# Kernel optimization log

Measured on AMD Instinct MI355X. Metric: run time of the kernel, lower is better.

The kernel has to match this reference:

```python
import jax, jax.numpy as jnp
import numpy as np

NUM_HEADS = 12
HEAD_DIM = 64
DIM = 768
ATTN_DIM = 768
SEQ = 4096


def _rotate_half(t):
    # split last dim in halves: (x1, x2) -> (-x2, x1)
    x1, x2 = jnp.split(t, 2, axis=-1)
    return jnp.concatenate([-x2, x1], axis=-1)


def _apply_rope(t, freqs):
    # t: [B,H,L,d], freqs: [1,1,L,d]
    return t * jnp.cos(freqs) + _rotate_half(t) * jnp.sin(freqs)


def setup_inputs() -> dict:
    key = jax.random.key(0)
    ks = jax.random.split(key, 8)
    x = jax.random.normal(ks[0], (1, SEQ, DIM), dtype=jnp.float32)
    # standard rotary frequencies: theta = pos * inv_freq, concatenated twice to head_dim
    inv_freq = 1.0 / (10000.0 ** (jnp.arange(0, HEAD_DIM, 2, dtype=jnp.float32) / HEAD_DIM))
    pos = jnp.arange(SEQ, dtype=jnp.float32)
    ang = pos[:, None] * inv_freq[None, :]                      # [L, d/2]
    rope = jnp.concatenate([ang, ang], axis=-1)[None, None]     # [1,1,L,d]
    s = 0.02
    Wq = jax.random.normal(ks[1], (ATTN_DIM, DIM), dtype=jnp.float32) * s
    Wk = jax.random.normal(ks[2], (ATTN_DIM, DIM), dtype=jnp.float32) * s
    Wv = jax.random.normal(ks[3], (ATTN_DIM, DIM), dtype=jnp.float32) * s
    Wo = jax.random.normal(ks[4], (DIM, ATTN_DIM), dtype=jnp.float32) * s
    bo = jnp.zeros((DIM,), dtype=jnp.float32)
    gamma = jnp.ones((DIM,), dtype=jnp.float32)
    beta = jnp.zeros((DIM,), dtype=jnp.float32)
    return {"x": x, "Wq": Wq, "Wk": Wk, "Wv": Wv, "Wo": Wo, "bo": bo,
            "gamma": gamma, "beta": beta, "rope": rope}


def reference(x, Wq, Wk, Wv, Wo, bo, gamma, beta, rope):
    B, L, D = x.shape
    residual = x
    # pre-LayerNorm
    mu = jnp.mean(x, axis=-1, keepdims=True)
    var = jnp.mean((x - mu) ** 2, axis=-1, keepdims=True)
    xn = (x - mu) * jax.lax.rsqrt(var + 1e-5) * gamma + beta

    def heads(t):  # [B,L,attn_dim] -> [B,H,L,d]
        return t.reshape(B, L, NUM_HEADS, HEAD_DIM).transpose(0, 2, 1, 3)

    q = heads(xn @ Wq.T)
    k = heads(xn @ Wk.T)
    v = heads(xn @ Wv.T)
    q = _apply_rope(q, rope)
    k = _apply_rope(k, rope)
    v = _apply_rope(v, rope)

    scale = HEAD_DIM ** -0.5
    dots = jnp.einsum('bhid,bhjd->bhij', q, k) * scale
    # causal mask: positions j > i masked
    i = jnp.arange(L)
    mask = i[:, None] < i[None, :]  # True where future
    neg = -jnp.finfo(dots.dtype).max
    dots = jnp.where(mask[None, None], neg, dots)
    attn_map = jax.nn.softmax(dots, axis=-1)

    o = jnp.einsum('bhij,bhjd->bhid', attn_map, v)
    o = o.transpose(0, 2, 1, 3).reshape(B, L, ATTN_DIM)
    out = o @ Wo.T + bo + residual
    return out, attn_map, dots
```

## Files before the change

### kernel.cpp

```cpp
#include <hip/hip_runtime.h>
#include <hip/hip_bf16.h>
#include <cfloat>
#include <cmath>

#define SEQ 4096
#define DIM 768
#define NH 12
#define HD 64
#define NEG_MASK (-0x1.FEp+127f)

typedef __attribute__((ext_vector_type(8))) short short8_t;
typedef __attribute__((ext_vector_type(4))) float f32x4;

static __device__ __forceinline__ unsigned short f2bf(float f) {
  __hip_bfloat16 h = __float2bfloat16(f);
  unsigned short u;
  __builtin_memcpy(&u, &h, 2);
  return u;
}

static __device__ __forceinline__ void st_nt(float* p, f32x4 v) {
  __builtin_nontemporal_store(v, (f32x4*)p);
}
static __device__ __forceinline__ f32x4 ld_lds4(const float* p) {
  return *(const f32x4*)p;
}

__global__ __launch_bounds__(256) void ln_kernel(const float* __restrict__ x,
    const float* __restrict__ gamma, const float* __restrict__ beta,
    unsigned short* __restrict__ xnb) {
  int row = blockIdx.x;
  const float* xr = x + (size_t)row * DIM;
  int t = threadIdx.x;
  float v0 = xr[t], v1 = xr[t + 256], v2 = xr[t + 512];
  float s = v0 + v1 + v2;
  float s2 = v0 * v0 + v1 * v1 + v2 * v2;
  for (int off = 32; off > 0; off >>= 1) {
    s += __shfl_down(s, off, 64);
    s2 += __shfl_down(s2, off, 64);
  }
  __shared__ float red[2][4];
  int wid = t >> 6;
  if ((t & 63) == 0) { red[0][wid] = s; red[1][wid] = s2; }
  __syncthreads();
  s = red[0][0] + red[0][1] + red[0][2] + red[0][3];
  s2 = red[1][0] + red[1][1] + red[1][2] + red[1][3];
  float mu = s * (1.0f / DIM);
  float var = s2 * (1.0f / DIM) - mu * mu;
  float rstd = rsqrtf(var + 1e-5f);
  unsigned short* xo = xnb + (size_t)row * DIM;
  xo[t]       = f2bf((v0 - mu) * rstd * gamma[t]       + beta[t]);
  xo[t + 256] = f2bf((v1 - mu) * rstd * gamma[t + 256] + beta[t + 256]);
  xo[t + 512] = f2bf((v2 - mu) * rstd * gamma[t + 512] + beta[t + 512]);
}

__global__ __launch_bounds__(256) void wcvt_kernel(const float* __restrict__ w0,
    const float* __restrict__ w1, const float* __restrict__ w2, const float* __restrict__ w3,
    unsigned short* __restrict__ o0, unsigned short* __restrict__ o1,
    unsigned short* __restrict__ o2, unsigned short* __restrict__ o3) {
  const float* src; unsigned short* dst;
  switch (blockIdx.y) {
    case 0: src = w0; dst = o0; break;
    case 1: src = w1; dst = o1; break;
    case 2: src = w2; dst = o2; break;
    default: src = w3; dst = o3; break;
  }
  size_t base = ((size_t)blockIdx.x * 256 + threadIdx.x) * 8;
  float4 a = *(const float4*)(src + base);
  float4 b = *(const float4*)(src + base + 4);
  ushort4 ua, ub;
  ua.x = f2bf(a.x); ua.y = f2bf(a.y); ua.z = f2bf(a.z); ua.w = f2bf(a.w);
  ub.x = f2bf(b.x); ub.y = f2bf(b.y); ub.z = f2bf(b.z); ub.w = f2bf(b.w);
  *(ushort4*)(dst + base) = ua;
  *(ushort4*)(dst + base + 4) = ub;
}

__global__ __launch_bounds__(256) void qkv_kernel(const unsigned short* __restrict__ xnb,
    const unsigned short* __restrict__ wqb, const unsigned short* __restrict__ wkb,
    const unsigned short* __restrict__ wvb, const float* __restrict__ ropes,
    unsigned short* __restrict__ qb, unsigned short* __restrict__ kb,
    unsigned short* __restrict__ vbT) {
  int z = blockIdx.z;
  const unsigned short* W = (z == 0) ? wqb : (z == 1) ? wkb : wvb;
  int h = blockIdx.y;
  int n0 = h * 64;
  int tid = threadIdx.x;
  int w = tid >> 6, l = tid & 63;
  int col_l = l & 15, rowg = l >> 4, kgrp = rowg * 8;
  int mbase = blockIdx.x * 64 + w * 16;

  f32x4 acc[4];
  #pragma unroll
  for (int g = 0; g < 4; g++) acc[g] = (f32x4){0.f, 0.f, 0.f, 0.f};

  for (int k0 = 0; k0 < DIM; k0 += 32) {
    short8_t a = *(const short8_t*)(xnb + (size_t)(mbase + col_l) * DIM + k0 + kgrp);
    #pragma unroll
    for (int g = 0; g < 4; g++) {
      short8_t bw = *(const short8_t*)(W + (size_t)(n0 + g * 16 + col_l) * DIM + k0 + kgrp);
      acc[g] = __builtin_amdgcn_mfma_f32_16x16x32_bf16(a, bw, acc[g], 0, 0, 0);
    }
  }

  float res[4][4];
  #pragma unroll
  for (int g = 0; g < 4; g++) {
    int d = g * 16 + col_l;
    #pragma unroll
    for (int r = 0; r < 4; r++) {
      int m = mbase + rowg * 4 + r;
      float f = ropes[(size_t)m * HD + d];
      float val = acc[g][r];
      float oth = acc[g ^ 2][r];
      float rot = (g < 2) ? -oth : oth;
      res[g][r] = val * cosf(f) + rot * sinf(f);
    }
  }

  if (z < 2) {
    unsigned short* dst = (z == 0) ? qb : kb;
    #pragma unroll
    for (int g = 0; g < 4; g++) {
      int d = g * 16 + col_l;
      #pragma unroll
      for (int r = 0; r < 4; r++)
        dst[((size_t)h * SEQ + mbase + rowg * 4 + r) * HD + d] = f2bf(res[g][r]);
    }
  } else {
    #pragma unroll
    for (int g = 0; g < 4; g++) {
      int d = g * 16 + col_l;
      ushort4 u;
      u.x = f2bf(res[g][0]); u.y = f2bf(res[g][1]);
      u.z = f2bf(res[g][2]); u.w = f2bf(res[g][3]);
      *(ushort4*)(vbT + ((size_t)h * HD + d) * SEQ + mbase + rowg * 4) = u;
    }
  }
}

__global__ __launch_bounds__(256, 4) void attn_fused(
    const unsigned short* __restrict__ qb, const unsigned short* __restrict__ kb,
    const unsigned short* __restrict__ vbT,
    float* __restrict__ dots, float* __restrict__ attnp, unsigned short* __restrict__ ob) {
  int band = (SEQ / 16 - 1) - blockIdx.x;
  int h = blockIdx.y;
  int i0 = band * 16;
  int jd = i0 >> 6;
  int tid = threadIdx.x;
  int w = tid >> 6, l = tid & 63;
  int col_l = l & 15, rg = l >> 4, kgrp = rg * 8;
  int c4 = col_l * 4;

  const unsigned short* qh = qb + (size_t)h * SEQ * HD;
  const unsigned short* kh = kb + (size_t)h * SEQ * HD;
  const unsigned short* vh = vbT + (size_t)h * HD * SEQ;
  size_t obase = (size_t)h * SEQ * SEQ;

  __shared__ float pt[4][16][68];
  __shared__ float stats[4][16][2];

  const unsigned short* qrow = qh + (size_t)(i0 + col_l) * HD + kgrp;
  short8_t aq0 = *(const short8_t*)(qrow);
  short8_t aq1 = *(const short8_t*)(qrow + 32);

  float mreg[4], lreg[4];
  #pragma unroll
  for (int r = 0; r < 4; r++) { mreg[r] = -FLT_MAX; lreg[r] = 0.f; }

  for (int jt = w; jt <= jd; jt += 4) {
    int j0 = jt * 64;
    f32x4 acc[4];
    #pragma unroll
    for (int b = 0; b < 4; b++) {
      const unsigned short* kr = kh + (size_t)(j0 + b * 16 + col_l) * HD + kgrp;
      short8_t bk0 = *(const short8_t*)(kr);
      short8_t bk1 = *(const short8_t*)(kr + 32);
      f32x4 z = {0.f, 0.f, 0.f, 0.f};
      acc[b] = __builtin_amdgcn_mfma_f32_16x16x32_bf16(aq0, bk0, z, 0, 0, 0);
      acc[b] = __builtin_amdgcn_mfma_f32_16x16x32_bf16(aq1, bk1, acc[b], 0, 0, 0);
    }
    bool diag = (jt == jd);
    #pragma unroll
    for (int b = 0; b < 4; b++) {
      int j = j0 + b * 16 + col_l;
      #pragma unroll
      for (int r = 0; r < 4; r++) {
        float s = acc[b][r] * 0.125f;
        acc[b][r] = (diag && j > i0 + rg * 4 + r) ? NEG_MASK : s;
      }
    }
    #pragma unroll
    for (int r = 0; r < 4; r++) {
      float tm = fmaxf(fmaxf(acc[0][r], acc[1][r]), fmaxf(acc[2][r], acc[3][r]));
      if (tm > -1e30f) {
        float nm = fmaxf(mreg[r], tm);
        lreg[r] = lreg[r] * __expf(mreg[r] - nm) +
                  __expf(acc[0][r] - nm) + __expf(acc[1][r] - nm) +
                  __expf(acc[2][r] - nm) + __expf(acc[3][r] - nm);
        mreg[r] = nm;
      }
    }
    #pragma unroll
    for (int b = 0; b < 4; b++)
      #pragma unroll
      for (int r = 0; r < 4; r++)
        pt[w][rg * 4 + r][b * 16 + col_l] = acc[b][r];
    #pragma unroll
    for (int e = 0; e < 4; e++) {
      f32x4 v = ld_lds4(&pt[w][e * 4 + rg][c4]);
      st_nt(dots + obase + (size_t)(i0 + e * 4 + rg) * SEQ + j0 + c4, v);
    }
  }

  #pragma unroll
  for (int r = 0; r < 4; r++) {
    float m = mreg[r], lv = lreg[r];
    #pragma unroll
    for (int off = 1; off < 16; off <<= 1) {
      float om = __shfl_xor(m, off, 16);
      float ol = __shfl_xor(lv, off, 16);
      float nm = fmaxf(m, om);
      lv = lv * __expf(m - nm) + ol * __expf(om - nm);
      m = nm;
    }
    mreg[r] = m; lreg[r] = lv;
  }
  if (col_l == 0) {
    #pragma unroll
    for (int r = 0; r < 4; r++) {
      stats[w][rg * 4 + r][0] = mreg[r];
      stats[w][rg * 4 + r][1] = lreg[r];
    }
  }
  __syncthreads();
  float M_[4], rl_[4];
  #pragma unroll
  for (int r = 0; r < 4; r++) {
    int row = rg * 4 + r;
    float m0 = stats[0][row][0], m1 = stats[1][row][0];
    float m2 = stats[2][row][0], m3 = stats[3][row][0];
    float mm = fmaxf(fmaxf(m0, m1), fmaxf(m2, m3));
    float L = stats[0][row][1] * __expf(m0 - mm) + stats[1][row][1] * __expf(m1 - mm) +
              stats[2][row][1] * __expf(m2 - mm) + stats[3][row][1] * __expf(m3 - mm);
    M_[r] = mm;
    rl_[r] = 1.0f / L;
  }

  f32x4 o[4];
  #pragma unroll
  for (int dg = 0; dg < 4; dg++) o[dg] = (f32x4){0.f, 0.f, 0.f, 0.f};

  for (int jt = w; jt <= jd; jt += 4) {
    int j0 = jt * 64;
    f32x4 acc[4];
    #pragma unroll
    for (int b = 0; b < 4; b++) {
      const unsigned short* kr = kh + (size_t)(j0 + b * 16 + col_l) * HD + kgrp;
      short8_t bk0 = *(const short8_t*)(kr);
      short8_t bk1 = *(const short8_t*)(kr + 32);
      f32x4 z = {0.f, 0.f, 0.f, 0.f};
      acc[b] = __builtin_amdgcn_mfma_f32_16x16x32_bf16(aq0, bk0, z, 0, 0, 0);
      acc[b] = __builtin_amdgcn_mfma_f32_16x16x32_bf16(aq1, bk1, acc[b], 0, 0, 0);
    }
    bool diag = (jt == jd);
    #pragma unroll
    for (int b = 0; b < 4; b++) {
      int j = j0 + b * 16 + col_l;
      #pragma unroll
      for (int r = 0; r < 4; r++) {
        float s = acc[b][r] * 0.125f;
        s = (diag && j > i0 + rg * 4 + r) ? NEG_MASK : s;
        float p = __expf(s - M_[r]) * rl_[r];
        pt[w][rg * 4 + r][b * 16 + col_l] = p;
      }
    }
    #pragma unroll
    for (int e = 0; e < 4; e++) {
      f32x4 v = ld_lds4(&pt[w][e * 4 + rg][c4]);
      st_nt(attnp + obase + (size_t)(i0 + e * 4 + rg) * SEQ + j0 + c4, v);
    }
    short8_t pa[2];
    #pragma unroll
    for (int ks = 0; ks < 2; ks++) {
      const float* src = &pt[w][col_l][ks * 32 + kgrp];
      f32x4 x0 = ld_lds4(src);
      f32x4 x1 = ld_lds4(src + 4);
      short8_t t;
      t[0] = (short)f2bf(x0.x); t[1] = (short)f2bf(x0.y);
      t[2] = (short)f2bf(x0.z); t[3] = (short)f2bf(x0.w);
      t[4] = (short)f2bf(x1.x); t[5] = (short)f2bf(x1.y);
      t[6] = (short)f2bf(x1.z); t[7] = (short)f2bf(x1.w);
      pa[ks] = t;
    }
    #pragma unroll
    for (int dg = 0; dg < 4; dg++) {
      const unsigned short* vr = vh + (size_t)(dg * 16 + col_l) * SEQ + j0 + kgrp;
      short8_t bv0 = *(const short8_t*)(vr);
      short8_t bv1 = *(const short8_t*)(vr + 32);
      o[dg] = __builtin_amdgcn_mfma_f32_16x16x32_bf16(pa[0], bv0, o[dg], 0, 0, 0);
      o[dg] = __builtin_amdgcn_mfma_f32_16x16x32_bf16(pa[1], bv1, o[dg], 0, 0, 0);
    }
  }

  {
    int c0 = (jd + 1) * 64;
    int nf4 = (SEQ - c0) >> 2;
    if (nf4 > 0) {
      f32x4 dm = (f32x4){NEG_MASK, NEG_MASK, NEG_MASK, NEG_MASK};
      f32x4 zz = (f32x4){0.f, 0.f, 0.f, 0.f};
      for (int r16 = 0; r16 < 16; r16++) {
        float* dr = dots  + obase + (size_t)(i0 + r16) * SEQ + c0;
        float* ar = attnp + obase + (size_t)(i0 + r16) * SEQ + c0;
        for (int c = tid; c < nf4; c += 256) {
          st_nt(dr + c * 4, dm);
          st_nt(ar + c * 4, zz);
        }
      }
    }
  }

  __syncthreads();
  #pragma unroll
  for (int dg = 0; dg < 4; dg++)
    #pragma unroll
    for (int r = 0; r < 4; r++)
      pt[w][rg * 4 + r][dg * 16 + col_l] = o[dg][r];
  __syncthreads();
  {
    int idx = tid * 4;
    int row = idx >> 6, col = idx & 63;
    f32x4 s = ld_lds4(&pt[0][row][col]);
    #pragma unroll
    for (int w2 = 1; w2 < 4; w2++) {
      f32x4 t = ld_lds4(&pt[w2][row][col]);
      s.x += t.x; s.y += t.y; s.z += t.z; s.w += t.w;
    }
    ushort4 u;
    u.x = f2bf(s.x); u.y = f2bf(s.y); u.z = f2bf(s.z); u.w = f2bf(s.w);
    *(ushort4*)(ob + (size_t)(i0 + row) * DIM + h * HD + col) = u;
  }
}

__global__ __launch_bounds__(256) void out_kernel(const unsigned short* __restrict__ ob,
    const unsigned short* __restrict__ wob, const float* __restrict__ bias,
    const float* __restrict__ resid, float* __restrict__ out) {
  int n0 = blockIdx.y * 64;
  int tid = threadIdx.x;
  int w = tid >> 6, l = tid & 63;
  int col_l = l & 15, rowg = l >> 4, kgrp = rowg * 8;
  int mbase = blockIdx.x * 64 + w * 16;

  f32x4 acc[4];
  #pragma unroll
  for (int g = 0; g < 4; g++) acc[g] = (f32x4){0.f, 0.f, 0.f, 0.f};

  for (int k0 = 0; k0 < DIM; k0 += 32) {
    short8_t a = *(const short8_t*)(ob + (size_t)(mbase + col_l) * DIM + k0 + kgrp);
    #pragma unroll
    for (int g = 0; g < 4; g++) {
      short8_t bw = *(const short8_t*)(wob + (size_t)(n0 + g * 16 + col_l) * DIM + k0 + kgrp);
      acc[g] = __builtin_amdgcn_mfma_f32_16x16x32_bf16(a, bw, acc[g], 0, 0, 0);
    }
  }
  #pragma unroll
  for (int g = 0; g < 4; g++) {
    int n = n0 + g * 16 + col_l;
    float bn = bias[n];
    #pragma unroll
    for (int r = 0; r < 4; r++) {
      int m = mbase + rowg * 4 + r;
      out[(size_t)m * DIM + n] = acc[g][r] + bn + resid[(size_t)m * DIM + n];
    }
  }
}

extern "C" void kernel_launch(void* const* d_in, const int* in_sizes, int n_in,
                              void* d_out, int out_size, void* d_ws, size_t ws_size,
                              hipStream_t stream) {
  const float* x     = (const float*)d_in[0];
  const float* Wq    = (const float*)d_in[1];
  const float* Wk    = (const float*)d_in[2];
  const float* Wv    = (const float*)d_in[3];
  const float* Wo    = (const float*)d_in[4];
  const float* bo    = (const float*)d_in[5];
  const float* gamma = (const float*)d_in[6];
  const float* beta  = (const float*)d_in[7];
  const float* rope  = (const float*)d_in[8];

  float* out  = (float*)d_out;
  float* attn = out + (size_t)SEQ * DIM;
  float* dots = attn + (size_t)NH * SEQ * SEQ;

  char* ws = (char*)d_ws;
  unsigned short* xnb = (unsigned short*)(ws);
  unsigned short* qb  = (unsigned short*)(ws + 6291456);
  unsigned short* kb  = (unsigned short*)(ws + 12582912);
  unsigned short* vbT = (unsigned short*)(ws + 18874368);
  unsigned short* ob  = (unsigned short*)(ws + 25165824);
  unsigned short* wqb = (unsigned short*)(ws + 31457280);
  unsigned short* wkb = (unsigned short*)(ws + 32636928);
  unsigned short* wvb = (unsigned short*)(ws + 33816576);
  unsigned short* wob = (unsigned short*)(ws + 34996224);

  ln_kernel<<<SEQ, 256, 0, stream>>>(x, gamma, beta, xnb);
  wcvt_kernel<<<dim3(288, 4), 256, 0, stream>>>(Wq, Wk, Wv, Wo, wqb, wkb, wvb, wob);
  qkv_kernel<<<dim3(SEQ / 64, NH, 3), 256, 0, stream>>>(xnb, wqb, wkb, wvb, rope, qb, kb, vbT);
  attn_fused<<<dim3(SEQ / 16, NH), 256, 0, stream>>>(qb, kb, vbT, dots, attn, ob);
  out_kernel<<<dim3(SEQ / 64, DIM / 64), 256, 0, stream>>>(ob, wob, bo, x, out);
}
```

Before: 563.7 us.

## Reuse stored dots in softmax pass instead of recomputing QK^T

The second pass no longer recomputes Q·K^T with MFMA. It re-reads the dots already written by the first pass, which now uses regular cached stores instead of nontemporal ones so the data may still sit in cache. The per-row max and reciprocal sum are computed once by one wave and shared through LDS, and the V loads are issued early to overlap with the exp work. The cost is re-reading a large fp32 dots band from memory, which only pays off if it hits L2 or MALL.

```diff
diff --git a/kernel.cpp b/kernel.cpp
--- a/kernel.cpp
+++ b/kernel.cpp
@@ -158,6 +158,7 @@
 
   __shared__ float pt[4][16][68];
   __shared__ float stats[4][16][2];
+  __shared__ float ml2[16][2];
 
   const unsigned short* qrow = qh + (size_t)(i0 + col_l) * HD + kgrp;
   short8_t aq0 = *(const short8_t*)(qrow);
@@ -208,7 +209,7 @@
     #pragma unroll
     for (int e = 0; e < 4; e++) {
       f32x4 v = ld_lds4(&pt[w][e * 4 + rg][c4]);
-      st_nt(dots + obase + (size_t)(i0 + e * 4 + rg) * SEQ + j0 + c4, v);
+      *(f32x4*)(dots + obase + (size_t)(i0 + e * 4 + rg) * SEQ + j0 + c4) = v;
     }
   }
 
@@ -233,17 +234,25 @@
     }
   }
   __syncthreads();
-  float M_[4], rl_[4];
-  #pragma unroll
-  for (int r = 0; r < 4; r++) {
-    int row = rg * 4 + r;
-    float m0 = stats[0][row][0], m1 = stats[1][row][0];
-    float m2 = stats[2][row][0], m3 = stats[3][row][0];
-    float mm = fmaxf(fmaxf(m0, m1), fmaxf(m2, m3));
-    float L = stats[0][row][1] * __expf(m0 - mm) + stats[1][row][1] * __expf(m1 - mm) +
-              stats[2][row][1] * __expf(m2 - mm) + stats[3][row][1] * __expf(m3 - mm);
-    M_[r] = mm;
-    rl_[r] = 1.0f / L;
+  if (w == 0 && col_l == 0) {
+    #pragma unroll
+    for (int r = 0; r < 4; r++) {
+      int row = rg * 4 + r;
+      float m0 = stats[0][row][0], m1 = stats[1][row][0];
+      float m2 = stats[2][row][0], m3 = stats[3][row][0];
+      float mm = fmaxf(fmaxf(m0, m1), fmaxf(m2, m3));
+      float L = stats[0][row][1] * __expf(m0 - mm) + stats[1][row][1] * __expf(m1 - mm) +
+                stats[2][row][1] * __expf(m2 - mm) + stats[3][row][1] * __expf(m3 - mm);
+      ml2[row][0] = mm;
+      ml2[row][1] = 1.0f / L;
+    }
+  }
+  __syncthreads();
+  float Mr[4], Rr[4];
+  #pragma unroll
+  for (int e = 0; e < 4; e++) {
+    Mr[e] = ml2[e * 4 + rg][0];
+    Rr[e] = ml2[e * 4 + rg][1];
   }
 
   f32x4 o[4];
@@ -252,32 +261,26 @@
 
   for (int jt = w; jt <= jd; jt += 4) {
     int j0 = jt * 64;
-    f32x4 acc[4];
-    #pragma unroll
-    for (int b = 0; b < 4; b++) {
-      const unsigned short* kr = kh + (size_t)(j0 + b * 16 + col_l) * HD + kgrp;
-      short8_t bk0 = *(const short8_t*)(kr);
-      short8_t bk1 = *(const short8_t*)(kr + 32);
-      f32x4 z = {0.f, 0.f, 0.f, 0.f};
-      acc[b] = __builtin_amdgcn_mfma_f32_16x16x32_bf16(aq0, bk0, z, 0, 0, 0);
-      acc[b] = __builtin_amdgcn_mfma_f32_16x16x32_bf16(aq1, bk1, acc[b], 0, 0, 0);
-    }
-    bool diag = (jt == jd);
-    #pragma unroll
-    for (int b = 0; b < 4; b++) {
-      int j = j0 + b * 16 + col_l;
-      #pragma unroll
-      for (int r = 0; r < 4; r++) {
-        float s = acc[b][r] * 0.125f;
-        s = (diag && j > i0 + rg * 4 + r) ? NEG_MASK : s;
-        float p = __expf(s - M_[r]) * rl_[r];
-        pt[w][rg * 4 + r][b * 16 + col_l] = p;
-      }
-    }
+    short8_t bv0[4], bv1[4];
+    #pragma unroll
+    for (int dg = 0; dg < 4; dg++) {
+      const unsigned short* vr = vh + (size_t)(dg * 16 + col_l) * SEQ + j0 + kgrp;
+      bv0[dg] = *(const short8_t*)(vr);
+      bv1[dg] = *(const short8_t*)(vr + 32);
+    }
+    f32x4 d4[4];
+    #pragma unroll
+    for (int e = 0; e < 4; e++)
+      d4[e] = *(const f32x4*)(dots + obase + (size_t)(i0 + e * 4 + rg) * SEQ + j0 + c4);
     #pragma unroll
     for (int e = 0; e < 4; e++) {
-      f32x4 v = ld_lds4(&pt[w][e * 4 + rg][c4]);
-      st_nt(attnp + obase + (size_t)(i0 + e * 4 + rg) * SEQ + j0 + c4, v);
+      f32x4 p;
+      p.x = __expf(d4[e].x - Mr[e]) * Rr[e];
+      p.y = __expf(d4[e].y - Mr[e]) * Rr[e];
+      p.z = __expf(d4[e].z - Mr[e]) * Rr[e];
+      p.w = __expf(d4[e].w - Mr[e]) * Rr[e];
+      st_nt(attnp + obase + (size_t)(i0 + e * 4 + rg) * SEQ + j0 + c4, p);
+      *(f32x4*)&pt[w][e * 4 + rg][c4] = p;
     }
     short8_t pa[2];
     #pragma unroll
@@ -294,11 +297,8 @@
     }
     #pragma unroll
     for (int dg = 0; dg < 4; dg++) {
-      const unsigned short* vr = vh + (size_t)(dg * 16 + col_l) * SEQ + j0 + kgrp;
-      short8_t bv0 = *(const short8_t*)(vr);
-      short8_t bv1 = *(const short8_t*)(vr + 32);
-      o[dg] = __builtin_amdgcn_mfma_f32_16x16x32_bf16(pa[0], bv0, o[dg], 0, 0, 0);
-      o[dg] = __builtin_amdgcn_mfma_f32_16x16x32_bf16(pa[1], bv1, o[dg], 0, 0, 0);
+      o[dg] = __builtin_amdgcn_mfma_f32_16x16x32_bf16(pa[0], bv0[dg], o[dg], 0, 0, 0);
+      o[dg] = __builtin_amdgcn_mfma_f32_16x16x32_bf16(pa[1], bv1[dg], o[dg], 0, 0, 0);
     }
   }
 
```

Result: slower. 634.5 us (+12.6%).
